# Performance work log

Measured on AMD Instinct MI355X. Metric: run time of the kernel, lower is better.

The kernel has to match this reference:

```python
import jax, jax.numpy as jnp
import numpy as np

HEADS = 8
DIM_HEAD = 64
TEMPERATURE = 0.5
ALPHA = 0.7


def _forward(x, grad, W_qkv, W_out, b_out):
    b, p, n, _ = x.shape
    h, dh = HEADS, DIM_HEAD
    qkv = x @ W_qkv                                   # (b,p,n,3*h*dh)
    q, k, v = jnp.split(qkv, 3, axis=-1)
    # 'b p n (h d) -> b p h n d'
    q = q.reshape(b, p, n, h, dh).transpose(0, 1, 3, 2, 4)
    k = k.reshape(b, p, n, h, dh).transpose(0, 1, 3, 2, 4)
    v = v.reshape(b, p, n, h, dh).transpose(0, 1, 3, 2, 4)
    kv = jnp.concatenate([k, v], axis=-1)             # (b,p,h,n,2*dh)
    w = int(n ** 0.5)
    topk = w * w // 25
    # grad-guided scoring (indices end up not affecting values: the torch code
    # gathers along the freshly-repeated axis, which is constant, so the gather
    # is exactly a broadcast of kv over topk; we still compute top_k faithfully)
    pos = jax.nn.softmax(grad / TEMPERATURE, axis=-1)
    neg = jax.nn.softmax(-grad / TEMPERATURE, axis=-1)
    grad_norm = ALPHA * pos + (1.0 - ALPHA) * (1.0 - neg)
    _vals, _idx = jax.lax.top_k(grad_norm, topk)      # (b,p,h,n,topk)
    kv_sel = jnp.broadcast_to(kv[:, :, :, :, None, :], (b, p, h, n, topk, 2 * dh))
    # torch: reshape(b*h, p, n, topk, 2dh) then flatten -> layout-scrambling reshape
    kv_sel = kv_sel.reshape(b * h * p, n, topk, 2 * dh)
    k_sel, v_sel = kv_sel[..., :dh], kv_sel[..., dh:]
    # '(n p) t k c -> (n t) p c k'
    k_sel = k_sel.reshape(b * h, p, n, topk, dh).transpose(0, 2, 1, 4, 3).reshape(b * h * n, p, dh, topk)
    # '(n p) t k c -> (n t) p k c'
    v_sel = v_sel.reshape(b * h, p, n, topk, dh).transpose(0, 2, 1, 3, 4).reshape(b * h * n, p, topk, dh)
    # q: (b,p,h,n,dh) -> reshape(b*h, p, n, dh) then 'n h t c -> (n t) h c'
    q2 = q.reshape(b * h, p, n, dh).transpose(0, 2, 1, 3).reshape(b * h * n, p, 1, dh)
    scale = dh ** -0.5
    attn = jax.nn.softmax((q2 * scale) @ k_sel, axis=-1)   # (b*h*n, p, 1, topk)
    o = (attn @ v_sel)[:, :, 0, :]                         # (b*h*n, p, dh)
    # '(n t) h k -> n h t k' with n=b*h
    o = o.reshape(b * h, n, p, dh).transpose(0, 2, 1, 3)   # (b*h, p, n, dh)
    o = jax.nn.gelu(o, approximate=False)                  # torch F.gelu (erf)
    # '(b h) p n d -> b p n (h d)'
    o = o.reshape(b, h, p, n, dh).transpose(0, 2, 3, 1, 4).reshape(b, p, n, h * dh)
    return o @ W_out + b_out                               # dropout p=0 -> identity


def setup_inputs() -> dict:
    key = jax.random.key(0)
    k0, k1, k2, k3 = jax.random.split(key, 4)
    b, p, n, dim = 2, 16, 256, 512
    h, dh = HEADS, DIM_HEAD
    inner = h * dh
    return {
        "x": jax.random.normal(k0, (b, p, n, dim), jnp.float32),
        "grad": jax.random.normal(k1, (b, p, h, n, n), jnp.float32),
        "W_qkv": jax.random.normal(k2, (dim, 3 * inner), jnp.float32) * 0.02,
        "W_out": jax.random.normal(k3, (inner, dim), jnp.float32) * 0.02,
        "b_out": jnp.zeros((dim,), jnp.float32),
    }


def reference(x, grad, W_qkv, W_out, b_out):
    return _forward(x, grad, W_qkv, W_out, b_out)
```

## Files before the change

kernel.cpp:

```cpp
#include <hip/hip_runtime.h>
#include <stdint.h>


typedef __bf16 bf16x8 __attribute__((ext_vector_type(8)));
typedef float f32x4 __attribute__((ext_vector_type(4)));
typedef unsigned short u16x8 __attribute__((ext_vector_type(8)));

#define HD __device__ __forceinline__

HD uint16_t f2bf(float f) {
  union { float f; uint32_t u; } v; v.f = f;
  uint32_t u = v.u;
  u += 0x7fffu + ((u >> 16) & 1u);
  return (uint16_t)(u >> 16);
}

HD void gll16(const void* g, void* l) {
  __builtin_amdgcn_global_load_lds(
      (__attribute__((address_space(1))) void*)g,
      (__attribute__((address_space(3))) void*)l, 16, 0, 0);
}

HD float gelu(float v) {
  float x = v * 0.70710678118654752440f;
  float ax = __builtin_fabsf(x);
  float t = __builtin_amdgcn_rcpf(1.0f + 0.47047f * ax);
  float poly = t * (0.3480242f + t * (-0.0958798f + t * 0.7478556f));
  float e = 1.0f - poly * __builtin_amdgcn_exp2f(-ax * ax * 1.44269504088896340736f);
  union { float f; uint32_t u; } ue, ux;
  ue.f = e; ux.f = x;
  ue.u = (ue.u & 0x7fffffffu) | (ux.u & 0x80000000u);
  return 0.5f * v * (1.0f + ue.f);
}

__global__ __launch_bounds__(256) void k_cvtx(
    const float* __restrict__ X, uint16_t* __restrict__ Xb) {
  const size_t i = ((size_t)blockIdx.x * 256 + threadIdx.x) * 8;
  f32x4 a = *(const f32x4*)(X + i);
  f32x4 b = *(const f32x4*)(X + i + 4);
  u16x8 o;
  o[0] = f2bf(a[0]); o[1] = f2bf(a[1]); o[2] = f2bf(a[2]); o[3] = f2bf(a[3]);
  o[4] = f2bf(b[0]); o[5] = f2bf(b[1]); o[6] = f2bf(b[2]); o[7] = f2bf(b[3]);
  *(u16x8*)(Xb + i) = o;
}

__global__ __launch_bounds__(256) void k_prep(
    const float* __restrict__ Wqkv, const float* __restrict__ Wout,
    uint16_t* __restrict__ WvT, uint16_t* __restrict__ WoT) {
  const float* in;
  uint16_t* out;
  int ldin, coloff;
  if (blockIdx.z == 0) { in = Wqkv; ldin = 1536; coloff = 1024; out = WvT; }
  else                 { in = Wout; ldin = 512;  coloff = 0;    out = WoT; }

  __shared__ uint16_t t[64][66];
  const int tid = threadIdx.x;
  const int tx = tid & 63;
  const int ty = tid >> 6;
  const int j0 = blockIdx.x * 64;
  const int k0 = blockIdx.y * 64;
#pragma unroll
  for (int r = 0; r < 16; ++r) {
    int k = ty * 16 + r;
    t[k][tx] = f2bf(in[(size_t)(k0 + k) * ldin + coloff + j0 + tx]);
  }
  __syncthreads();
#pragma unroll
  for (int r = 0; r < 16; ++r) {
    int j = ty * 16 + r;
    out[(size_t)(j0 + j) * 512 + k0 + tx] = t[tx][j];
  }
}

__global__ __launch_bounds__(256) void k_gemm1(
    const uint16_t* __restrict__ Xb,
    const uint16_t* __restrict__ WT,
    uint16_t* __restrict__ Zlin) {
  __shared__ __align__(16) uint16_t As[2][4][64][8];
  __shared__ __align__(16) uint16_t Bs[2][4][128][8];

  const int tid = threadIdx.x;
  const int lane = tid & 63;
  const int wid = tid >> 6;
  const int wm = wid >> 1;
  const int wn = wid & 1;
  const int tm = blockIdx.y * 64;
  const int tn = blockIdx.x * 128;

  f32x4 acc[2][4];
  const f32x4 zero = {0.f, 0.f, 0.f, 0.f};
#pragma unroll
  for (int i = 0; i < 2; ++i)
#pragma unroll
    for (int j = 0; j < 4; ++j) acc[i][j] = zero;

  auto stage = [&](int kk, int buf) {
    gll16(Xb + (size_t)(tm + lane) * 512 + kk * 32 + wid * 8,
          &As[buf][wid][0][0]);
#pragma unroll
    for (int s = 0; s < 2; ++s) {
      int t = wid + 4 * s;
      int kc = t >> 1;
      int cb = (t & 1) * 64;
      gll16(WT + (size_t)(tn + cb + lane) * 512 + kk * 32 + kc * 8,
            &Bs[buf][kc][cb][0]);
    }
  };

  stage(0, 0);
  __syncthreads();

  const int lr = lane & 15;
  const int lk = lane >> 4;

#pragma unroll 2
  for (int kk = 0; kk < 16; ++kk) {
    const int cur = kk & 1;
    if (kk + 1 < 16) stage(kk + 1, cur ^ 1);
    bf16x8 a[2], b[4];
#pragma unroll
    for (int mi = 0; mi < 2; ++mi)
      a[mi] = *(const bf16x8*)&As[cur][lk][wm * 32 + mi * 16 + lr][0];
#pragma unroll
    for (int nj = 0; nj < 4; ++nj)
      b[nj] = *(const bf16x8*)&Bs[cur][lk][wn * 64 + nj * 16 + lr][0];
#pragma unroll
    for (int mi = 0; mi < 2; ++mi)
#pragma unroll
      for (int nj = 0; nj < 4; ++nj)
        acc[mi][nj] = __builtin_amdgcn_mfma_f32_16x16x32_bf16(
            a[mi], b[nj], acc[mi][nj], 0, 0, 0);
    __syncthreads();
  }

#pragma unroll
  for (int mi = 0; mi < 2; ++mi)
#pragma unroll
    for (int nj = 0; nj < 4; ++nj)
#pragma unroll
      for (int r = 0; r < 4; ++r) {
        int m = tm + wm * 32 + mi * 16 + lk * 4 + r;
        int j = tn + wn * 64 + nj * 16 + lr;
        Zlin[(size_t)m * 512 + j] = f2bf(gelu(acc[mi][nj][r]));
      }
}

__global__ __launch_bounds__(256) void k_gemm_bias(
    const uint16_t* __restrict__ Zlin,
    const uint16_t* __restrict__ WT,
    const float* __restrict__ bias,
    float* __restrict__ Y) {
  __shared__ __align__(16) uint16_t As[2][4][64][8];
  __shared__ __align__(16) uint16_t Bs[2][4][128][8];

  const int tid = threadIdx.x;
  const int lane = tid & 63;
  const int wid = tid >> 6;
  const int wm = wid >> 1;
  const int wn = wid & 1;
  const int tm = blockIdx.y * 64;
  const int tn = blockIdx.x * 128;

  f32x4 acc[2][4];
  const f32x4 zero = {0.f, 0.f, 0.f, 0.f};
#pragma unroll
  for (int i = 0; i < 2; ++i)
#pragma unroll
    for (int j = 0; j < 4; ++j) acc[i][j] = zero;

  const int m2 = tm + lane;
  const int bi = m2 >> 12;
  const int pp = (m2 >> 8) & 15;
  const int ni = m2 & 255;
  const int mbase = bi * 4096 + (pp >> 3) * 256 + ni;
  const int jbase = (pp & 7) * 64;

  auto stage = [&](int kk, int buf) {
    int k2 = kk * 32 + wid * 8;
    int q = k2 >> 6;
    int di = k2 & 63;
    gll16(Zlin + (size_t)(mbase + q * 512) * 512 + jbase + di,
          &As[buf][wid][0][0]);
#pragma unroll
    for (int s = 0; s < 2; ++s) {
      int t = wid + 4 * s;
      int kc = t >> 1;
      int cb = (t & 1) * 64;
      gll16(WT + (size_t)(tn + cb + lane) * 512 + kk * 32 + kc * 8,
            &Bs[buf][kc][cb][0]);
    }
  };

  stage(0, 0);
  __syncthreads();

  const int lr = lane & 15;
  const int lk = lane >> 4;

#pragma unroll 2
  for (int kk = 0; kk < 16; ++kk) {
    const int cur = kk & 1;
    if (kk + 1 < 16) stage(kk + 1, cur ^ 1);
    bf16x8 a[2], b[4];
#pragma unroll
    for (int mi = 0; mi < 2; ++mi)
      a[mi] = *(const bf16x8*)&As[cur][lk][wm * 32 + mi * 16 + lr][0];
#pragma unroll
    for (int nj = 0; nj < 4; ++nj)
      b[nj] = *(const bf16x8*)&Bs[cur][lk][wn * 64 + nj * 16 + lr][0];
#pragma unroll
    for (int mi = 0; mi < 2; ++mi)
#pragma unroll
      for (int nj = 0; nj < 4; ++nj)
        acc[mi][nj] = __builtin_amdgcn_mfma_f32_16x16x32_bf16(
            a[mi], b[nj], acc[mi][nj], 0, 0, 0);
    __syncthreads();
  }

#pragma unroll
  for (int mi = 0; mi < 2; ++mi)
#pragma unroll
    for (int nj = 0; nj < 4; ++nj) {
      int j = tn + wn * 64 + nj * 16 + lr;
      float bj = bias[j];
#pragma unroll
      for (int r = 0; r < 4; ++r) {
        int m = tm + wm * 32 + mi * 16 + lk * 4 + r;
        Y[(size_t)m * 512 + j] = acc[mi][nj][r] + bj;
      }
    }
}

extern "C" void kernel_launch(void* const* d_in, const int* in_sizes, int n_in,
                              void* d_out, int out_size, void* d_ws, size_t ws_size,
                              hipStream_t stream) {
  const float* x    = (const float*)d_in[0];
  const float* Wqkv = (const float*)d_in[2];
  const float* Wout = (const float*)d_in[3];
  const float* bout = (const float*)d_in[4];
  float* Y = (float*)d_out;

  uint16_t* WvT = (uint16_t*)d_ws;
  uint16_t* WoT = WvT + 512 * 512;
  uint16_t* Z   = WoT + 512 * 512;
  uint16_t* Xb  = Z + 8192 * 512;

  dim3 tb(256);
  k_cvtx<<<dim3(2048), tb, 0, stream>>>(x, Xb);
  k_prep<<<dim3(8, 8, 2), tb, 0, stream>>>(Wqkv, Wout, WvT, WoT);
  k_gemm1<<<dim3(4, 128), tb, 0, stream>>>(Xb, WvT, Z);
  k_gemm_bias<<<dim3(4, 128), tb, 0, stream>>>(Z, WoT, bout, Y);
}
```

Measured before the change: 47.95 us.

## Fuse fp32-to-bf16 conversion of X into first GEMM and widen its N tile

Removes the separate X conversion kernel. The first GEMM now stages fp32 X tiles directly into LDS and converts them to bf16 fragments in registers. The GEMM tile also grows to cover all 512 output columns per block, so each block reads X only once. This drops one launch and the bf16 round trip of X, but cuts the grid to 128 blocks, raises LDS and register use (32 accumulators per thread), and adds conversion work inside the inner loop.

```diff
diff --git a/kernel.cpp b/kernel.cpp
--- a/kernel.cpp
+++ b/kernel.cpp
@@ -4,7 +4,6 @@
 
 typedef __bf16 bf16x8 __attribute__((ext_vector_type(8)));
 typedef float f32x4 __attribute__((ext_vector_type(4)));
-typedef unsigned short u16x8 __attribute__((ext_vector_type(8)));
 
 #define HD __device__ __forceinline__
 
@@ -19,6 +18,17 @@
   __builtin_amdgcn_global_load_lds(
       (__attribute__((address_space(1))) void*)g,
       (__attribute__((address_space(3))) void*)l, 16, 0, 0);
+}
+
+HD bf16x8 cvt_frag(const float* p) {
+  f32x4 f0 = *(const f32x4*)p;
+  f32x4 f1 = *(const f32x4*)(p + 4);
+  bf16x8 r;
+  r[0] = (__bf16)f0[0]; r[1] = (__bf16)f0[1];
+  r[2] = (__bf16)f0[2]; r[3] = (__bf16)f0[3];
+  r[4] = (__bf16)f1[0]; r[5] = (__bf16)f1[1];
+  r[6] = (__bf16)f1[2]; r[7] = (__bf16)f1[3];
+  return r;
 }
 
 HD float gelu(float v) {
@@ -33,17 +43,6 @@
   return 0.5f * v * (1.0f + ue.f);
 }
 
-__global__ __launch_bounds__(256) void k_cvtx(
-    const float* __restrict__ X, uint16_t* __restrict__ Xb) {
-  const size_t i = ((size_t)blockIdx.x * 256 + threadIdx.x) * 8;
-  f32x4 a = *(const f32x4*)(X + i);
-  f32x4 b = *(const f32x4*)(X + i + 4);
-  u16x8 o;
-  o[0] = f2bf(a[0]); o[1] = f2bf(a[1]); o[2] = f2bf(a[2]); o[3] = f2bf(a[3]);
-  o[4] = f2bf(b[0]); o[5] = f2bf(b[1]); o[6] = f2bf(b[2]); o[7] = f2bf(b[3]);
-  *(u16x8*)(Xb + i) = o;
-}
-
 __global__ __launch_bounds__(256) void k_prep(
     const float* __restrict__ Wqkv, const float* __restrict__ Wout,
     uint16_t* __restrict__ WvT, uint16_t* __restrict__ WoT) {
@@ -73,36 +72,36 @@
 }
 
 __global__ __launch_bounds__(256) void k_gemm1(
-    const uint16_t* __restrict__ Xb,
+    const float* __restrict__ X,
     const uint16_t* __restrict__ WT,
     uint16_t* __restrict__ Zlin) {
-  __shared__ __align__(16) uint16_t As[2][4][64][8];
-  __shared__ __align__(16) uint16_t Bs[2][4][128][8];
+  __shared__ __align__(16) float As[2][2][64][16];
+  __shared__ __align__(16) uint16_t Bs[2][4][512][8];
 
   const int tid = threadIdx.x;
   const int lane = tid & 63;
   const int wid = tid >> 6;
-  const int wm = wid >> 1;
-  const int wn = wid & 1;
-  const int tm = blockIdx.y * 64;
-  const int tn = blockIdx.x * 128;
-
-  f32x4 acc[2][4];
+  const int tm = blockIdx.x * 64;
+
+  f32x4 acc[4][8];
   const f32x4 zero = {0.f, 0.f, 0.f, 0.f};
 #pragma unroll
-  for (int i = 0; i < 2; ++i)
-#pragma unroll
-    for (int j = 0; j < 4; ++j) acc[i][j] = zero;
+  for (int i = 0; i < 4; ++i)
+#pragma unroll
+    for (int j = 0; j < 8; ++j) acc[i][j] = zero;
 
   auto stage = [&](int kk, int buf) {
-    gll16(Xb + (size_t)(tm + lane) * 512 + kk * 32 + wid * 8,
-          &As[buf][wid][0][0]);
 #pragma unroll
     for (int s = 0; s < 2; ++s) {
+      gll16(X + (size_t)(tm + wid * 16 + (lane >> 2)) * 512 + kk * 32 + s * 16 + (lane & 3) * 4,
+            &As[buf][s][wid * 16][0]);
+    }
+#pragma unroll
+    for (int s = 0; s < 8; ++s) {
       int t = wid + 4 * s;
-      int kc = t >> 1;
-      int cb = (t & 1) * 64;
-      gll16(WT + (size_t)(tn + cb + lane) * 512 + kk * 32 + kc * 8,
+      int kc = t & 3;
+      int cb = (t >> 2) * 64;
+      gll16(WT + (size_t)(cb + lane) * 512 + kk * 32 + kc * 8,
             &Bs[buf][kc][cb][0]);
     }
   };
@@ -113,34 +112,33 @@
   const int lr = lane & 15;
   const int lk = lane >> 4;
 
-#pragma unroll 2
   for (int kk = 0; kk < 16; ++kk) {
     const int cur = kk & 1;
     if (kk + 1 < 16) stage(kk + 1, cur ^ 1);
-    bf16x8 a[2], b[4];
-#pragma unroll
-    for (int mi = 0; mi < 2; ++mi)
-      a[mi] = *(const bf16x8*)&As[cur][lk][wm * 32 + mi * 16 + lr][0];
-#pragma unroll
-    for (int nj = 0; nj < 4; ++nj)
-      b[nj] = *(const bf16x8*)&Bs[cur][lk][wn * 64 + nj * 16 + lr][0];
-#pragma unroll
-    for (int mi = 0; mi < 2; ++mi)
-#pragma unroll
-      for (int nj = 0; nj < 4; ++nj)
+    bf16x8 a[4], b[8];
+#pragma unroll
+    for (int mi = 0; mi < 4; ++mi)
+      a[mi] = cvt_frag(&As[cur][lk >> 1][mi * 16 + lr][(lk & 1) * 8]);
+#pragma unroll
+    for (int nj = 0; nj < 8; ++nj)
+      b[nj] = *(const bf16x8*)&Bs[cur][lk][wid * 128 + nj * 16 + lr][0];
+#pragma unroll
+    for (int mi = 0; mi < 4; ++mi)
+#pragma unroll
+      for (int nj = 0; nj < 8; ++nj)
         acc[mi][nj] = __builtin_amdgcn_mfma_f32_16x16x32_bf16(
             a[mi], b[nj], acc[mi][nj], 0, 0, 0);
     __syncthreads();
   }
 
 #pragma unroll
-  for (int mi = 0; mi < 2; ++mi)
-#pragma unroll
-    for (int nj = 0; nj < 4; ++nj)
+  for (int mi = 0; mi < 4; ++mi)
+#pragma unroll
+    for (int nj = 0; nj < 8; ++nj)
 #pragma unroll
       for (int r = 0; r < 4; ++r) {
-        int m = tm + wm * 32 + mi * 16 + lk * 4 + r;
-        int j = tn + wn * 64 + nj * 16 + lr;
+        int m = tm + mi * 16 + lk * 4 + r;
+        int j = wid * 128 + nj * 16 + lr;
         Zlin[(size_t)m * 512 + j] = f2bf(gelu(acc[mi][nj][r]));
       }
 }
@@ -243,11 +241,9 @@
   uint16_t* WvT = (uint16_t*)d_ws;
   uint16_t* WoT = WvT + 512 * 512;
   uint16_t* Z   = WoT + 512 * 512;
-  uint16_t* Xb  = Z + 8192 * 512;
 
   dim3 tb(256);
-  k_cvtx<<<dim3(2048), tb, 0, stream>>>(x, Xb);
   k_prep<<<dim3(8, 8, 2), tb, 0, stream>>>(Wqkv, Wout, WvT, WoT);
-  k_gemm1<<<dim3(4, 128), tb, 0, stream>>>(Xb, WvT, Z);
+  k_gemm1<<<dim3(128), tb, 0, stream>>>(x, WvT, Z);
   k_gemm_bias<<<dim3(4, 128), tb, 0, stream>>>(Z, WoT, bout, Y);
 }
```

Measured after the change: 71.06 us. 48.2% more time.
